# Kernel tuning notes

Hardware: AMD Instinct MI355X
Metric: run time of the kernel (lower is better)

## Reference

```python
import jax, jax.numpy as jnp
import numpy as np

N = 100000
E = 1600000
IN_C = 128
HID = 32
H1 = 4
OUT_C = 32
H2 = 1
NEG_SLOPE = 0.2


def setup_inputs() -> dict:
    key = jax.random.key(0)
    ks = jax.random.split(key, 12)
    g = 0.1  # glorot-ish scale
    return {
        "x": jax.random.normal(ks[0], (N, IN_C), jnp.float32),
        "edge_index": jax.random.randint(ks[1], (2, E), 0, N, jnp.int64),
        "W1": jax.random.normal(ks[2], (IN_C, H1 * HID), jnp.float32) * g,
        "att_src1": jax.random.normal(ks[3], (H1, HID), jnp.float32) * g,
        "att_dst1": jax.random.normal(ks[4], (H1, HID), jnp.float32) * g,
        "b1": jnp.zeros((H1 * HID,), jnp.float32),
        "W2": jax.random.normal(ks[5], (H1 * HID, H2 * OUT_C), jnp.float32) * g,
        "att_src2": jax.random.normal(ks[6], (H2, OUT_C), jnp.float32) * g,
        "att_dst2": jax.random.normal(ks[7], (H2, OUT_C), jnp.float32) * g,
        "b2": jnp.zeros((H2 * OUT_C,), jnp.float32),
    }


def gat_conv(x, src, dst, W, att_src, att_dst, bias, heads, ch):
    n = x.shape[0]
    h = (x @ W).reshape(n, heads, ch)                      # [N,H,C]
    a_src = jnp.sum(h * att_src, axis=-1)                  # [N,H]
    a_dst = jnp.sum(h * att_dst, axis=-1)                  # [N,H]
    e = jax.nn.leaky_relu(a_src[src] + a_dst[dst], NEG_SLOPE)  # [E,H]
    # segment softmax over destination neighborhoods
    m = jax.ops.segment_max(e, dst, num_segments=n)        # [N,H]
    ex = jnp.exp(e - m[dst])
    denom = jax.ops.segment_sum(ex, dst, num_segments=n)   # [N,H]
    alpha = ex / (denom[dst] + 1e-16)                      # [E,H]
    msg = h[src] * alpha[:, :, None]                       # [E,H,C]
    out = jax.ops.segment_sum(msg, dst, num_segments=n)    # [N,H,C]
    return out.reshape(n, heads * ch) + bias


def reference(x, edge_index, W1, att_src1, att_dst1, b1, W2, att_src2, att_dst2, b2):
    # PyG GATConv add_self_loops=True
    loops = jnp.arange(N, dtype=edge_index.dtype)
    src = jnp.concatenate([edge_index[0], loops])
    dst = jnp.concatenate([edge_index[1], loops])
    # dropout is a no-op at inference
    h = gat_conv(x, src, dst, W1, att_src1, att_dst1, b1, H1, HID)
    h = jax.nn.relu(h)
    out = gat_conv(h, src, dst, W2, att_src2, att_dst2, b2, H2, OUT_C)
    return out
```

## Files before the change

kernel.cpp:

```cpp
#include <hip/hip_runtime.h>
#include <hip/hip_bf16.h>


#define NSLOPE 0.2f
#define GSTRIDE 136
#define NB_MAX 400
#define CHUNK 4096
#define CAP 5632

typedef __attribute__((ext_vector_type(8))) short short8;
typedef __attribute__((ext_vector_type(4))) float floatx4;

__device__ __forceinline__ float leaky(float v) { return v > 0.f ? v : NSLOPE * v; }

__device__ __forceinline__ unsigned short f2bf(float f) {
  __hip_bfloat16 b = __float2bfloat16(f);
  return *reinterpret_cast<unsigned short*>(&b);
}
__device__ __forceinline__ float bf2f(unsigned int u) {
  return __uint_as_float(u << 16);
}
__device__ __forceinline__ unsigned int pack2(float a, float b) {
  return (unsigned int)f2bf(a) | ((unsigned int)f2bf(b) << 16);
}

__global__ __launch_bounds__(256, 2) void fused1_kernel(
    const float* __restrict__ x, const float* __restrict__ W,
    const float* __restrict__ atts, const float* __restrict__ attd,
    unsigned short* __restrict__ h, float* __restrict__ asrc, float* __restrict__ adst,
    int n, int g1blocks,
    const int* __restrict__ ei, int* __restrict__ bincur,
    unsigned int* __restrict__ staging, int E, int ET, int nb) {
  __shared__ __align__(16) unsigned char smem[70656];
  const int tid = threadIdx.x;

  if (blockIdx.x < g1blocks) {
    unsigned short* xs = (unsigned short*)smem;
    unsigned short* wt = (unsigned short*)(smem + 34816);
    float* att_s = (float*)(smem + 69632);
    float* att_d = (float*)(smem + 70144);
    const int row0 = blockIdx.x * 128;

    if (tid < 128) { att_s[tid] = atts[tid]; att_d[tid] = attd[tid]; }

    const float4* w4 = (const float4*)W;
#pragma unroll
    for (int i = 0; i < 16; i++) {
      int idx = tid + i * 256;
      int k = idx >> 5, n0 = (idx & 31) * 4;
      float4 v = w4[idx];
      float vv[4] = {v.x, v.y, v.z, v.w};
#pragma unroll
      for (int jj = 0; jj < 4; jj++) {
        int j = (jj + tid) & 3;
        wt[(n0 + j) * GSTRIDE + k] = f2bf(vv[j]);
      }
    }

    const float4* x4 = (const float4*)x;
#pragma unroll
    for (int i = 0; i < 16; i++) {
      int idx = tid + i * 256;
      int r = idx >> 5, c4 = idx & 31;
      float4 v = make_float4(0.f, 0.f, 0.f, 0.f);
      if (row0 + r < n) v = x4[(size_t)(row0 + r) * 32 + c4];
      unsigned int* p = (unsigned int*)&xs[r * GSTRIDE + c4 * 4];
      p[0] = pack2(v.x, v.y);
      p[1] = pack2(v.z, v.w);
    }
    __syncthreads();

    const int l = tid & 63;
    const int w = tid >> 6;
    const int mrow = l & 15;
    const int q = l >> 4;
    floatx4 acc[2][8];
#pragma unroll
    for (int mt = 0; mt < 2; mt++)
#pragma unroll
      for (int nt = 0; nt < 8; nt++) acc[mt][nt] = (floatx4){0.f, 0.f, 0.f, 0.f};

#pragma unroll
    for (int ks = 0; ks < 4; ks++) {
      const int k0 = ks * 32 + q * 8;
      short8 a0 = *(const short8*)&xs[(w * 32 + mrow) * GSTRIDE + k0];
      short8 a1 = *(const short8*)&xs[(w * 32 + 16 + mrow) * GSTRIDE + k0];
#pragma unroll
      for (int nt = 0; nt < 8; nt++) {
        short8 b = *(const short8*)&wt[(nt * 16 + mrow) * GSTRIDE + k0];
        acc[0][nt] = __builtin_amdgcn_mfma_f32_16x16x32_bf16(a0, b, acc[0][nt], 0, 0, 0);
        acc[1][nt] = __builtin_amdgcn_mfma_f32_16x16x32_bf16(a1, b, acc[1][nt], 0, 0, 0);
      }
    }
    __syncthreads();

#pragma unroll
    for (int mt = 0; mt < 2; mt++)
#pragma unroll
      for (int nt = 0; nt < 8; nt++)
#pragma unroll
        for (int i = 0; i < 4; i++) {
          int r = w * 32 + mt * 16 + q * 4 + i;
          xs[r * GSTRIDE + nt * 16 + mrow] = f2bf(acc[mt][nt][i]);
        }
    __syncthreads();

#pragma unroll
    for (int i = 0; i < 8; i++) {
      int idx = tid + i * 256;
      int r = idx >> 4, c8 = (idx & 15) * 8;
      if (row0 + r < n) {
        unsigned int* p = (unsigned int*)&xs[r * GSTRIDE + c8];
        uint4 v = make_uint4(p[0], p[1], p[2], p[3]);
        *(uint4*)(h + (size_t)(row0 + r) * 128 + c8) = v;
      }
    }

#pragma unroll
    for (int rr = 0; rr < 2; rr++) {
      int row = (tid >> 2) + rr * 64;
      int head = tid & 3;
      float ss = 0.f, sd = 0.f;
#pragma unroll
      for (int c = 0; c < 32; c++) {
        int cr = (c + tid) & 31;
        float hv = bf2f(xs[row * GSTRIDE + head * 32 + cr]);
        ss += hv * att_s[head * 32 + cr];
        sd += hv * att_d[head * 32 + cr];
      }
      if (row0 + row < n) {
        asrc[(size_t)(row0 + row) * 4 + head] = ss;
        adst[(size_t)(row0 + row) * 4 + head] = sd;
      }
    }
  } else {
    int* hist  = (int*)smem;
    int* run   = (int*)(smem + 1600);
    int* rbase = (int*)(smem + 3200);
    const int base = (blockIdx.x - g1blocks) * CHUNK;
    for (int i = tid; i < nb; i += 256) { hist[i] = 0; run[i] = 0; }
    __syncthreads();
    int se[16], de[16];
#pragma unroll
    for (int j = 0; j < 16; j++) {
      int idx = base + j * 256 + tid;
      if (idx < ET) {
        if (idx < E) { se[j] = ei[idx]; de[j] = ei[E + idx]; }
        else         { se[j] = de[j] = idx - E; }
        atomicAdd(&hist[de[j] >> 8], 1);
      } else de[j] = -1;
    }
    __syncthreads();
    for (int i = tid; i < nb; i += 256)
      rbase[i] = hist[i] ? (i * CAP + atomicAdd(&bincur[i], hist[i])) : 0;
    __syncthreads();
#pragma unroll
    for (int j = 0; j < 16; j++) {
      if (de[j] >= 0) {
        int b = de[j] >> 8;
        int ofs = atomicAdd(&run[b], 1);
        staging[(size_t)rbase[b] + ofs] =
            (unsigned)se[j] | ((unsigned)(de[j] & 255) << 17);
      }
    }
  }
}

__global__ __launch_bounds__(1024) void binB_kernel(const unsigned int* __restrict__ staging,
                                                    const int* __restrict__ bincur,
                                                    int* __restrict__ rowbeg,
                                                    int* __restrict__ rowend,
                                                    int* __restrict__ bucket, int n) {
  __shared__ int cnt[256];
  __shared__ int cur[256];
  const int b = blockIdx.x;
  const int t = threadIdx.x;
  const int d0 = b << 8;
  const int nd = min(256, n - d0);
  const int base = b * CAP;
  const int rcnt = bincur[b];
  if (t < 256) cnt[t] = 0;
  __syncthreads();
  for (int j = t; j < rcnt; j += 1024) {
    unsigned int r = staging[(size_t)base + j];
    atomicAdd(&cnt[r >> 17], 1);
  }
  __syncthreads();
  int v = 0;
  if (t < 256) { v = cnt[t]; cur[t] = v; }
  __syncthreads();
  for (int off = 1; off < 256; off <<= 1) {
    int add = (t < 256 && t >= off) ? cur[t - off] : 0;
    __syncthreads();
    if (t < 256) cur[t] += add;
    __syncthreads();
  }
  if (t < 256) {
    int start = base + cur[t] - v;
    if (t < nd) { rowbeg[d0 + t] = start; rowend[d0 + t] = start + v; }
    cur[t] = start;
  }
  __syncthreads();
  for (int j = t; j < rcnt; j += 1024) {
    unsigned int r = staging[(size_t)base + j];
    int pos = atomicAdd(&cur[r >> 17], 1);
    bucket[pos] = (int)(r & 0x1FFFFu);
  }
}

__global__ __launch_bounds__(256) void g1_kernel(const int* __restrict__ rowbeg,
                                                 const int* __restrict__ rowend,
                                                 const int* __restrict__ bucket,
                                                 const float* __restrict__ asrc,
                                                 const float* __restrict__ adst,
                                                 const unsigned int* __restrict__ h,
                                                 const float* __restrict__ b1,
                                                 const float* __restrict__ W2,
                                                 const float* __restrict__ atts2,
                                                 const float* __restrict__ attd2,
                                                 unsigned short* __restrict__ h2,
                                                 float* __restrict__ asrc2,
                                                 float* __restrict__ adst2,
                                                 int n) {
  __shared__ __align__(16) float W2ld[128 * 32];
  __shared__ __align__(16) float xvld[4][128];
  const int tid = threadIdx.x;
  {
    const float4* w4 = (const float4*)W2;
    float4* wl = (float4*)W2ld;
#pragma unroll
    for (int i = 0; i < 4; i++) wl[tid + i * 256] = w4[tid + i * 256];
  }
  __syncthreads();

  const int lane = tid & 63;
  const int g = lane >> 3;
  const int l8 = lane & 7;
  const int head = l8 >> 1;
  const int wv = tid >> 6;
  const int d = blockIdx.x * 4 + wv;
  if (d >= n) return;
  const float ad = adst[(size_t)d * 4 + head];
  const int beg = rowbeg[d], end = rowend[d];
  float num[16];
#pragma unroll
  for (int j = 0; j < 16; j++) num[j] = 0.f;
  float den = 0.f;

  int i = beg + g;
  if (i < end) {
    int s = bucket[i];
    for (;;) {
      float a = asrc[(size_t)s * 4 + head];
      const uint4* hp = (const uint4*)(h + (size_t)s * 64 + l8 * 8);
      uint4 h0 = hp[0];
      uint4 h1v = hp[1];
      int i2 = i + 8;
      int s2 = (i2 < end) ? bucket[i2] : 0;
      float w = __expf(leaky(a + ad));
      den += w;
      num[0]  += w * bf2f(h0.x & 0xffffu);  num[1]  += w * bf2f(h0.x >> 16);
      num[2]  += w * bf2f(h0.y & 0xffffu);  num[3]  += w * bf2f(h0.y >> 16);
      num[4]  += w * bf2f(h0.z & 0xffffu);  num[5]  += w * bf2f(h0.z >> 16);
      num[6]  += w * bf2f(h0.w & 0xffffu);  num[7]  += w * bf2f(h0.w >> 16);
      num[8]  += w * bf2f(h1v.x & 0xffffu); num[9]  += w * bf2f(h1v.x >> 16);
      num[10] += w * bf2f(h1v.y & 0xffffu); num[11] += w * bf2f(h1v.y >> 16);
      num[12] += w * bf2f(h1v.z & 0xffffu); num[13] += w * bf2f(h1v.z >> 16);
      num[14] += w * bf2f(h1v.w & 0xffffu); num[15] += w * bf2f(h1v.w >> 16);
      if (i2 >= end) break;
      i = i2; s = s2;
    }
  }
#pragma unroll
  for (int j = 0; j < 16; j++) {
    num[j] += __shfl_xor(num[j], 8, 64);
    num[j] += __shfl_xor(num[j], 16, 64);
    num[j] += __shfl_xor(num[j], 32, 64);
  }
  den += __shfl_xor(den, 8, 64);
  den += __shfl_xor(den, 16, 64);
  den += __shfl_xor(den, 32, 64);
  const float inv = 1.f / (den + 1e-16f);
  if (g == 0) {
    const float4* b14 = (const float4*)b1;
    float4* xp = (float4*)&xvld[wv][l8 * 16];
#pragma unroll
    for (int k = 0; k < 4; k++) {
      float4 bb = b14[l8 * 4 + k];
      xp[k] = make_float4(fmaxf(num[k * 4 + 0] * inv + bb.x, 0.f),
                          fmaxf(num[k * 4 + 1] * inv + bb.y, 0.f),
                          fmaxf(num[k * 4 + 2] * inv + bb.z, 0.f),
                          fmaxf(num[k * 4 + 3] * inv + bb.w, 0.f));
    }
  }
  const int ocq = lane & 7;
  const int cb = lane >> 3;
  float p0 = 0.f, p1 = 0.f, p2 = 0.f, p3 = 0.f;
#pragma unroll
  for (int cc = 0; cc < 16; cc++) {
    int c = cb * 16 + cc;
    float xc = xvld[wv][c];
    float4 w4 = *(const float4*)&W2ld[c * 32 + ocq * 4];
    p0 += xc * w4.x; p1 += xc * w4.y; p2 += xc * w4.z; p3 += xc * w4.w;
  }
  p0 += __shfl_xor(p0, 8, 64); p0 += __shfl_xor(p0, 16, 64); p0 += __shfl_xor(p0, 32, 64);
  p1 += __shfl_xor(p1, 8, 64); p1 += __shfl_xor(p1, 16, 64); p1 += __shfl_xor(p1, 32, 64);
  p2 += __shfl_xor(p2, 8, 64); p2 += __shfl_xor(p2, 16, 64); p2 += __shfl_xor(p2, 32, 64);
  p3 += __shfl_xor(p3, 8, 64); p3 += __shfl_xor(p3, 16, 64); p3 += __shfl_xor(p3, 32, 64);
  if (cb == 0) {
    *(uint2*)(h2 + (size_t)d * 32 + ocq * 4) = make_uint2(pack2(p0, p1), pack2(p2, p3));
  }
  float4 as4 = ((const float4*)atts2)[ocq];
  float4 ad4 = ((const float4*)attd2)[ocq];
  float s2 = p0 * as4.x + p1 * as4.y + p2 * as4.z + p3 * as4.w;
  float t2 = p0 * ad4.x + p1 * ad4.y + p2 * ad4.z + p3 * ad4.w;
  s2 += __shfl_xor(s2, 1, 64); s2 += __shfl_xor(s2, 2, 64); s2 += __shfl_xor(s2, 4, 64);
  t2 += __shfl_xor(t2, 1, 64); t2 += __shfl_xor(t2, 2, 64); t2 += __shfl_xor(t2, 4, 64);
  if (lane == 0) { asrc2[d] = s2; adst2[d] = t2; }
}

__global__ __launch_bounds__(256) void g2_kernel(const int* __restrict__ rowbeg,
                                                 const int* __restrict__ rowend,
                                                 const int* __restrict__ bucket,
                                                 const float* __restrict__ asrc,
                                                 const float* __restrict__ adst,
                                                 const unsigned int* __restrict__ h2,
                                                 const float* __restrict__ b2,
                                                 float* __restrict__ out, int n) {
  const int lane = threadIdx.x & 63;
  const int g = lane >> 3;
  const int l8 = lane & 7;
  const int d = blockIdx.x * 4 + (threadIdx.x >> 6);
  if (d >= n) return;
  const float ad = adst[d];
  const int beg = rowbeg[d], end = rowend[d];
  float num[4];
#pragma unroll
  for (int j = 0; j < 4; j++) num[j] = 0.f;
  float den = 0.f;

  int i = beg + g;
  if (i < end) {
    int s = bucket[i];
    for (;;) {
      float a = asrc[s];
      uint2 hv = *(const uint2*)(h2 + (size_t)s * 16 + l8 * 2);
      int i2 = i + 8;
      int s2 = (i2 < end) ? bucket[i2] : 0;
      float w = __expf(leaky(a + ad));
      den += w;
      num[0] += w * bf2f(hv.x & 0xffffu); num[1] += w * bf2f(hv.x >> 16);
      num[2] += w * bf2f(hv.y & 0xffffu); num[3] += w * bf2f(hv.y >> 16);
      if (i2 >= end) break;
      i = i2; s = s2;
    }
  }
#pragma unroll
  for (int j = 0; j < 4; j++) {
    num[j] += __shfl_xor(num[j], 8, 64);
    num[j] += __shfl_xor(num[j], 16, 64);
    num[j] += __shfl_xor(num[j], 32, 64);
  }
  den += __shfl_xor(den, 8, 64);
  den += __shfl_xor(den, 16, 64);
  den += __shfl_xor(den, 32, 64);
  if (g == 0) {
    float inv = 1.f / (den + 1e-16f);
    float4 bb = ((const float4*)b2)[l8];
    *(float4*)(out + (size_t)d * 32 + l8 * 4) =
        make_float4(num[0] * inv + bb.x, num[1] * inv + bb.y,
                    num[2] * inv + bb.z, num[3] * inv + bb.w);
  }
}

extern "C" void kernel_launch(void* const* d_in, const int* in_sizes, int n_in,
                              void* d_out, int out_size, void* d_ws, size_t ws_size,
                              hipStream_t stream) {
  const float* x = (const float*)d_in[0];
  const int* ei = (const int*)d_in[1];
  const float* W1 = (const float*)d_in[2];
  const float* atts1 = (const float*)d_in[3];
  const float* attd1 = (const float*)d_in[4];
  const float* b1 = (const float*)d_in[5];
  const float* W2 = (const float*)d_in[6];
  const float* atts2 = (const float*)d_in[7];
  const float* attd2 = (const float*)d_in[8];
  const float* b2 = (const float*)d_in[9];
  float* out = (float*)d_out;

  const int N = in_sizes[0] / 128;
  const int E = in_sizes[1] / 2;
  const int ET = E + N;
  const int NB = (N + 255) >> 8;
  const int NCH = (ET + CHUNK - 1) / CHUNK;
  const int G1B = (N + 127) / 128;

  float* wsf = (float*)d_ws;
  float* asrc1 = wsf;
  float* adst1 = asrc1 + (size_t)N * 4;
  float* asrc2 = adst1 + (size_t)N * 4;
  float* adst2 = asrc2 + (size_t)N;
  unsigned short* h1 = (unsigned short*)(adst2 + (size_t)N);
  unsigned short* h2 = h1 + (size_t)N * 128;
  int* rowbeg = (int*)(h2 + (size_t)N * 32);
  int* rowend = rowbeg + N;
  int* bucket = rowend + N;
  unsigned int* staging = (unsigned int*)(bucket + (size_t)NB * CAP);
  int* bincur = (int*)(staging + (size_t)NB * CAP);

  hipMemsetAsync(bincur, 0, NB * sizeof(int), stream);
  fused1_kernel<<<G1B + NCH, 256, 0, stream>>>(x, W1, atts1, attd1, h1, asrc1, adst1,
                                               N, G1B, ei, bincur, staging, E, ET, NB);
  binB_kernel<<<NB, 1024, 0, stream>>>(staging, bincur, rowbeg, rowend, bucket, N);
  g1_kernel<<<(N + 3) / 4, 256, 0, stream>>>(rowbeg, rowend, bucket, asrc1, adst1,
                                             (const unsigned int*)h1, b1,
                                             W2, atts2, attd2, h2, asrc2, adst2, N);
  g2_kernel<<<(N + 3) / 4, 256, 0, stream>>>(rowbeg, rowend, bucket, asrc2, adst2,
                                             (const unsigned int*)h2, b2, out, N);
}
```

Measured before the change: 316.6 us.

## Drop shared-memory W2 staging in g1; read bf16 W2 from global per lane

The fused first kernel now converts W2 to bf16 once into a workspace buffer. g1 no longer copies W2 into LDS with a block-wide barrier per block. Instead, each lane uses its post-aggregation num values directly and reads bf16 W2 rows from global/L2, with shuffle reductions reorganised to match. This removes LDS staging, the barrier and the xvld round trip, raising occupancy, in exchange for more global weight loads per wave and bf16 precision on W2.

```diff
diff --git a/kernel.cpp b/kernel.cpp
--- a/kernel.cpp
+++ b/kernel.cpp
@@ -30,7 +30,8 @@
     unsigned short* __restrict__ h, float* __restrict__ asrc, float* __restrict__ adst,
     int n, int g1blocks,
     const int* __restrict__ ei, int* __restrict__ bincur,
-    unsigned int* __restrict__ staging, int E, int ET, int nb) {
+    unsigned int* __restrict__ staging, int E, int ET, int nb,
+    const float* __restrict__ W2src, unsigned short* __restrict__ w2p) {
   __shared__ __align__(16) unsigned char smem[70656];
   const int tid = threadIdx.x;
 
@@ -134,6 +135,10 @@
       }
     }
   } else {
+    if (blockIdx.x == g1blocks) {
+#pragma unroll
+      for (int i = 0; i < 16; i++) w2p[tid + i * 256] = f2bf(W2src[tid + i * 256]);
+    }
     int* hist  = (int*)smem;
     int* run   = (int*)(smem + 1600);
     int* rbase = (int*)(smem + 3200);
@@ -215,30 +220,18 @@
                                                  const float* __restrict__ adst,
                                                  const unsigned int* __restrict__ h,
                                                  const float* __restrict__ b1,
-                                                 const float* __restrict__ W2,
+                                                 const unsigned short* __restrict__ w2p,
                                                  const float* __restrict__ atts2,
                                                  const float* __restrict__ attd2,
                                                  unsigned short* __restrict__ h2,
                                                  float* __restrict__ asrc2,
                                                  float* __restrict__ adst2,
                                                  int n) {
-  __shared__ __align__(16) float W2ld[128 * 32];
-  __shared__ __align__(16) float xvld[4][128];
-  const int tid = threadIdx.x;
-  {
-    const float4* w4 = (const float4*)W2;
-    float4* wl = (float4*)W2ld;
-#pragma unroll
-    for (int i = 0; i < 4; i++) wl[tid + i * 256] = w4[tid + i * 256];
-  }
-  __syncthreads();
-
-  const int lane = tid & 63;
+  const int lane = threadIdx.x & 63;
   const int g = lane >> 3;
   const int l8 = lane & 7;
   const int head = l8 >> 1;
-  const int wv = tid >> 6;
-  const int d = blockIdx.x * 4 + wv;
+  const int d = blockIdx.x * 4 + (threadIdx.x >> 6);
   if (d >= n) return;
   const float ad = adst[(size_t)d * 4 + head];
   const int beg = rowbeg[d], end = rowend[d];
@@ -281,41 +274,46 @@
   den += __shfl_xor(den, 16, 64);
   den += __shfl_xor(den, 32, 64);
   const float inv = 1.f / (den + 1e-16f);
-  if (g == 0) {
-    const float4* b14 = (const float4*)b1;
-    float4* xp = (float4*)&xvld[wv][l8 * 16];
-#pragma unroll
-    for (int k = 0; k < 4; k++) {
-      float4 bb = b14[l8 * 4 + k];
-      xp[k] = make_float4(fmaxf(num[k * 4 + 0] * inv + bb.x, 0.f),
-                          fmaxf(num[k * 4 + 1] * inv + bb.y, 0.f),
-                          fmaxf(num[k * 4 + 2] * inv + bb.z, 0.f),
-                          fmaxf(num[k * 4 + 3] * inv + bb.w, 0.f));
-    }
-  }
-  const int ocq = lane & 7;
-  const int cb = lane >> 3;
+  const float4* b14 = (const float4*)b1;
+#pragma unroll
+  for (int k = 0; k < 4; k++) {
+    float4 bb = b14[l8 * 4 + k];
+    num[k * 4 + 0] = fmaxf(num[k * 4 + 0] * inv + bb.x, 0.f);
+    num[k * 4 + 1] = fmaxf(num[k * 4 + 1] * inv + bb.y, 0.f);
+    num[k * 4 + 2] = fmaxf(num[k * 4 + 2] * inv + bb.z, 0.f);
+    num[k * 4 + 3] = fmaxf(num[k * 4 + 3] * inv + bb.w, 0.f);
+  }
   float p0 = 0.f, p1 = 0.f, p2 = 0.f, p3 = 0.f;
-#pragma unroll
-  for (int cc = 0; cc < 16; cc++) {
-    int c = cb * 16 + cc;
-    float xc = xvld[wv][c];
-    float4 w4 = *(const float4*)&W2ld[c * 32 + ocq * 4];
-    p0 += xc * w4.x; p1 += xc * w4.y; p2 += xc * w4.z; p3 += xc * w4.w;
-  }
-  p0 += __shfl_xor(p0, 8, 64); p0 += __shfl_xor(p0, 16, 64); p0 += __shfl_xor(p0, 32, 64);
-  p1 += __shfl_xor(p1, 8, 64); p1 += __shfl_xor(p1, 16, 64); p1 += __shfl_xor(p1, 32, 64);
-  p2 += __shfl_xor(p2, 8, 64); p2 += __shfl_xor(p2, 16, 64); p2 += __shfl_xor(p2, 32, 64);
-  p3 += __shfl_xor(p3, 8, 64); p3 += __shfl_xor(p3, 16, 64); p3 += __shfl_xor(p3, 32, 64);
-  if (cb == 0) {
-    *(uint2*)(h2 + (size_t)d * 32 + ocq * 4) = make_uint2(pack2(p0, p1), pack2(p2, p3));
-  }
-  float4 as4 = ((const float4*)atts2)[ocq];
-  float4 ad4 = ((const float4*)attd2)[ocq];
+  const uint2* wq = (const uint2*)w2p;
+#pragma unroll 1
+  for (int cc4 = 0; cc4 < 4; cc4++) {
+    uint2 wv0 = wq[(l8 * 16 + cc4 * 4 + 0) * 8 + g];
+    uint2 wv1 = wq[(l8 * 16 + cc4 * 4 + 1) * 8 + g];
+    uint2 wv2 = wq[(l8 * 16 + cc4 * 4 + 2) * 8 + g];
+    uint2 wv3 = wq[(l8 * 16 + cc4 * 4 + 3) * 8 + g];
+#pragma unroll
+    for (int j = 0; j < 4; j++) {
+      uint2 wv_ = (j == 0) ? wv0 : (j == 1) ? wv1 : (j == 2) ? wv2 : wv3;
+      float xcv = num[cc4 * 4 + j];
+      p0 += xcv * bf2f(wv_.x & 0xffffu);
+      p1 += xcv * bf2f(wv_.x >> 16);
+      p2 += xcv * bf2f(wv_.y & 0xffffu);
+      p3 += xcv * bf2f(wv_.y >> 16);
+    }
+  }
+  p0 += __shfl_xor(p0, 1, 64); p0 += __shfl_xor(p0, 2, 64); p0 += __shfl_xor(p0, 4, 64);
+  p1 += __shfl_xor(p1, 1, 64); p1 += __shfl_xor(p1, 2, 64); p1 += __shfl_xor(p1, 4, 64);
+  p2 += __shfl_xor(p2, 1, 64); p2 += __shfl_xor(p2, 2, 64); p2 += __shfl_xor(p2, 4, 64);
+  p3 += __shfl_xor(p3, 1, 64); p3 += __shfl_xor(p3, 2, 64); p3 += __shfl_xor(p3, 4, 64);
+  if (l8 == 0) {
+    *(uint2*)(h2 + (size_t)d * 32 + g * 4) = make_uint2(pack2(p0, p1), pack2(p2, p3));
+  }
+  float4 as4 = ((const float4*)atts2)[g];
+  float4 ad4 = ((const float4*)attd2)[g];
   float s2 = p0 * as4.x + p1 * as4.y + p2 * as4.z + p3 * as4.w;
   float t2 = p0 * ad4.x + p1 * ad4.y + p2 * ad4.z + p3 * ad4.w;
-  s2 += __shfl_xor(s2, 1, 64); s2 += __shfl_xor(s2, 2, 64); s2 += __shfl_xor(s2, 4, 64);
-  t2 += __shfl_xor(t2, 1, 64); t2 += __shfl_xor(t2, 2, 64); t2 += __shfl_xor(t2, 4, 64);
+  s2 += __shfl_xor(s2, 8, 64); s2 += __shfl_xor(s2, 16, 64); s2 += __shfl_xor(s2, 32, 64);
+  t2 += __shfl_xor(t2, 8, 64); t2 += __shfl_xor(t2, 16, 64); t2 += __shfl_xor(t2, 32, 64);
   if (lane == 0) { asrc2[d] = s2; adst2[d] = t2; }
 }
 
@@ -407,14 +405,16 @@
   int* bucket = rowend + N;
   unsigned int* staging = (unsigned int*)(bucket + (size_t)NB * CAP);
   int* bincur = (int*)(staging + (size_t)NB * CAP);
+  unsigned short* w2p = (unsigned short*)(bincur + NB_MAX);
 
   hipMemsetAsync(bincur, 0, NB * sizeof(int), stream);
   fused1_kernel<<<G1B + NCH, 256, 0, stream>>>(x, W1, atts1, attd1, h1, asrc1, adst1,
-                                               N, G1B, ei, bincur, staging, E, ET, NB);
+                                               N, G1B, ei, bincur, staging, E, ET, NB,
+                                               W2, w2p);
   binB_kernel<<<NB, 1024, 0, stream>>>(staging, bincur, rowbeg, rowend, bucket, N);
   g1_kernel<<<(N + 3) / 4, 256, 0, stream>>>(rowbeg, rowend, bucket, asrc1, adst1,
                                              (const unsigned int*)h1, b1,
-                                             W2, atts2, attd2, h2, asrc2, adst2, N);
+                                             w2p, atts2, attd2, h2, asrc2, adst2, N);
   g2_kernel<<<(N + 3) / 4, 256, 0, stream>>>(rowbeg, rowend, bucket, asrc2, adst2,
                                              (const unsigned int*)h2, b2, out, N);
 }
```

Result: slower. 422.4 us (+33.4%).
